# Kernel optimization log

Measured on AMD Instinct MI355X. Metric: run time of the kernel, lower is better.

The kernel has to match this reference:

```python
import jax, jax.numpy as jnp
import numpy as np
from jax import lax

B, N, C, H, W, D, BEV = 2, 6, 64, 128, 352, 48, 64


def _make_buffers():
    # depths: linspace(1,100,D) -> used with shape (1,1,D,1)
    depths = jnp.linspace(1.0, 100.0, D).reshape(1, 1, D, 1)
    y, x = jnp.meshgrid(jnp.arange(H), jnp.arange(W), indexing='ij')
    xy1 = jnp.stack((x.flatten(), y.flatten(), jnp.ones(H * W)), axis=0).astype(jnp.float32)  # (3, H*W)
    return depths, xy1


def setup_inputs() -> dict:
    key = jax.random.key(0)
    ks = jax.random.split(key, 8)
    image_features = jax.random.normal(ks[0], (B * N, C, H, W), jnp.float32)
    # realistic invertible pinhole intrinsics embedded in 4x4
    fx = 500.0 + 10.0 * jax.random.normal(ks[1], (B, N))
    fy = 500.0 + 10.0 * jax.random.normal(ks[2], (B, N))
    K = jnp.tile(jnp.eye(4, dtype=jnp.float32), (B, N, 1, 1))
    K = K.at[..., 0, 0].set(fx).at[..., 1, 1].set(fy)
    K = K.at[..., 0, 2].set(W / 2.0).at[..., 1, 2].set(H / 2.0)
    extrinsics = jnp.tile(jnp.eye(4, dtype=jnp.float32), (B, N, 1, 1)) + 0.01 * jax.random.normal(ks[3], (B, N, 4, 4))
    view_attention = jnp.ones((1, N, 1, H, W), jnp.float32)
    depth_attention = jnp.ones((1, D, 1, 1), jnp.float32)
    # kaiming-normal conv weights (fan_in mode, relu gain sqrt(2))
    c1w = jax.random.normal(ks[4], (BEV, 3, 3, 3), jnp.float32) * np.sqrt(2.0 / (3 * 9))
    c1b = jnp.zeros((BEV,), jnp.float32)
    c2w = jax.random.normal(ks[5], (BEV, BEV, 3, 3), jnp.float32) * np.sqrt(2.0 / (BEV * 9))
    c2b = jnp.zeros((BEV,), jnp.float32)
    bn1_g = jnp.ones((BEV,), jnp.float32); bn1_b = jnp.zeros((BEV,), jnp.float32)
    bn2_g = jnp.ones((BEV,), jnp.float32); bn2_b = jnp.zeros((BEV,), jnp.float32)
    depths, xy1 = _make_buffers()
    return dict(image_features=image_features, intrinsics=K, extrinsics=extrinsics,
                view_attention=view_attention, depth_attention=depth_attention,
                c1w=c1w, c1b=c1b, bn1_g=bn1_g, bn1_b=bn1_b,
                c2w=c2w, c2b=c2b, bn2_g=bn2_g, bn2_b=bn2_b,
                depths=depths, xy1=xy1)


def _conv3x3(x, w, b):
    y = lax.conv_general_dilated(x, w, (1, 1), 'SAME',
                                 dimension_numbers=('NCHW', 'OIHW', 'NCHW'))
    return y + b.reshape(1, -1, 1, 1)


def _bn_train(x, g, b, eps=1e-5):
    # torch BatchNorm2d in training mode: biased batch stats over (B,H,W)
    m = x.mean(axis=(0, 2, 3), keepdims=True)
    v = x.var(axis=(0, 2, 3), keepdims=True)
    return g.reshape(1, -1, 1, 1) * (x - m) * lax.rsqrt(v + eps) + b.reshape(1, -1, 1, 1)


def reference(image_features, intrinsics, extrinsics, view_attention, depth_attention,
              c1w, c1b, bn1_g, bn1_b, c2w, c2b, bn2_g, bn2_b, depths, xy1):
    BN = B * N
    # ---- lift ----
    K3 = intrinsics.reshape(BN, 4, 4)[:, :3, :3]
    Kinv = jnp.linalg.inv(K3)                          # (BN,3,3)
    rays = jnp.einsum('bij,jp->bip', Kinv, xy1)        # (BN,3,H*W)
    # depths (1,1,D,1) * rays (BN,3,1,HW) -> (BN,3,D,HW), then the original's
    # .view(B,N,3,H,W,D) (a raw row-major reshape, reproduced faithfully)
    pc = (depths * rays[:, :, None, :]).reshape(B, N, 3, H, W, D)
    # (depth_probs in the original is computed then discarded; omitted)
    # ---- splat (fused weighted reduction over N and D) ----
    da = jax.nn.softmax(depth_attention, axis=1).reshape(D)       # (D,)
    va = jax.nn.softmax(view_attention, axis=1)[0, :, 0]          # (N,H,W)
    bev_features = jnp.einsum('bnchwd,d,nhw->bchw', pc, da, va)   # (B,3,H,W)
    h = jax.nn.relu(_bn_train(_conv3x3(bev_features, c1w, c1b), bn1_g, bn1_b))
    bev = jax.nn.relu(_bn_train(_conv3x3(h, c2w, c2b), bn2_g, bn2_b))
    return pc, bev
```

## Files before the change

### kernel.cpp

```cpp
#include <hip/hip_runtime.h>

#define W_ 352
#define H_ 128
#define HW 45056
#define D_ 48
#define B_ 2
#define N_ 6
#define DHW (D_*HW)
#define PC_SIZE (36*DHW)
#define BHW (B_*HW)
#define BEVN (B_*64*HW)

#define WS_KINV 0
#define WS_SUM1 192
#define WS_SQ1  256
#define WS_SUM2 448
#define WS_SQ2  512

#define NBN_BLK (BEVN/2048)
#define NPC_BLK (PC_SIZE/1024)

typedef unsigned short ushort_t;
typedef __attribute__((ext_vector_type(8))) short bf16x8;
typedef __attribute__((ext_vector_type(4))) float f32x4;
typedef __attribute__((ext_vector_type(8))) unsigned short u16x8;

static __device__ inline ushort_t f2bf(float f) {
    union { float f; unsigned u; } v; v.f = f;
    unsigned r = v.u + 0x7FFF + ((v.u >> 16) & 1);
    return (ushort_t)(r >> 16);
}
static __device__ inline float bf2f(ushort_t u) {
    union { unsigned u; float f; } v; v.u = ((unsigned)u) << 16; return v.f;
}
static __device__ inline void invert3x3(const float* __restrict__ M, float* __restrict__ o) {
    float a = M[0], b = M[1], c = M[2];
    float d = M[4], e = M[5], f = M[6];
    float g = M[8], h = M[9], ii = M[10];
    float det = a*(e*ii - f*h) - b*(d*ii - f*g) + c*(d*h - e*g);
    float inv = 1.f / det;
    o[0] = (e*ii - f*h)*inv; o[1] = (c*h - b*ii)*inv; o[2] = (b*f - c*e)*inv;
    o[3] = (f*g - d*ii)*inv; o[4] = (a*ii - c*g)*inv; o[5] = (c*d - a*f)*inv;
    o[6] = (d*h - e*g)*inv;  o[7] = (b*g - a*h)*inv;  o[8] = (a*e - b*d)*inv;
}

static __device__ inline void pc_write(int pcblk, const float* __restrict__ ws,
                                       const float* __restrict__ depths,
                                       float* __restrict__ out) {
    int f = pcblk * 1024 + (int)threadIdx.x * 4;
    int bnc = f / DHW;
    int r1  = f - bnc * DHW;
    int d   = r1 / HW;
    int p   = r1 - d * HW;
    int y   = p / W_;
    int x   = p - y * W_;
    float ka = ws[WS_KINV + bnc * 3 + 0];
    float kb = ws[WS_KINV + bnc * 3 + 1];
    float kc = ws[WS_KINV + bnc * 3 + 2];
    float dep = depths[d];
    float base = fmaf(kb, (float)y, kc);
    f32x4 v;
    v.x = dep * fmaf(ka, (float)(x + 0), base);
    v.y = dep * fmaf(ka, (float)(x + 1), base);
    v.z = dep * fmaf(ka, (float)(x + 2), base);
    v.w = dep * fmaf(ka, (float)(x + 3), base);
    __builtin_nontemporal_store(v, (f32x4*)(out + f));
}

__global__ __launch_bounds__(256) void k_fused1(const float* __restrict__ K4,
                                                const float* __restrict__ datt,
                                                const float* __restrict__ vatt,
                                                const float* __restrict__ depths,
                                                const float* __restrict__ w1,
                                                const float* __restrict__ b1,
                                                const float* __restrict__ w2,
                                                float* __restrict__ ws,
                                                ushort_t* __restrict__ h1pm,
                                                ushort_t* __restrict__ packedW) {
    int bid = blockIdx.x, tid = threadIdx.x;
    if (bid >= 352) {
        int e = (bid - 352) * 256 + tid;
        int tap = e >> 12;
        int r   = e & 4095;
        int n   = r >> 6, k = r & 63;
        int slot = (k >> 3) ^ (n & 7);
        packedW[tap * 4096 + n * 64 + slot * 8 + (k & 7)] = f2bf(w2[(n * 64 + k) * 9 + tap]);
        return;
    }
    if (bid == 0) {
        for (int i = 192 + tid; i < 576; i += 256) ws[i] = 0.f;
        if (tid >= 128 && tid < 140)
            invert3x3(K4 + (tid - 128) * 16, ws + WS_KINV + (tid - 128) * 9);
    }
    __shared__ float sBev[3][10][34];
    __shared__ float wl[64 * 27];
    __shared__ float sDep[48], sDa[48], sKinv[54];

    int b  = bid / 176;
    int t0 = bid - b * 176;
    int ty = t0 / 11, tx = t0 - ty * 11;
    int y0 = ty * 8, x0 = tx * 32;

    if (tid < 48) sDep[tid] = depths[tid];
    if (tid >= 64 && tid < 70) invert3x3(K4 + (b * 6 + tid - 64) * 16, sKinv + (tid - 64) * 9);
    if (tid == 192) {
        float mx = -1e30f;
        for (int k = 0; k < D_; k++) mx = fmaxf(mx, datt[k]);
        float s = 0.f, e[D_];
        for (int k = 0; k < D_; k++) { e[k] = expf(datt[k] - mx); s += e[k]; }
        float invs = 1.f / s;
        for (int k = 0; k < D_; k++) sDa[k] = e[k] * invs;
    }
    for (int i = tid; i < 64 * 27; i += 256) wl[i] = w1[i];
    __syncthreads();

    for (int idx = tid; idx < 340; idx += 256) {
        int hy = idx / 34, hx = idx - hy * 34;
        int py = y0 + hy - 1, px = x0 + hx - 1;
        float a0 = 0.f, a1 = 0.f, a2 = 0.f;
        if ((unsigned)py < H_ && (unsigned)px < W_) {
            int pix = py * W_ + px;
            float va[N_]; float mx = -1e30f;
            for (int n = 0; n < N_; n++) { va[n] = vatt[n * HW + pix]; mx = fmaxf(mx, va[n]); }
            float s = 0.f;
            for (int n = 0; n < N_; n++) { va[n] = expf(va[n] - mx); s += va[n]; }
            float invs = 1.f / s;
            int q0 = pix * 48;
            int d = q0 / HW;
            int p = q0 - d * HW;
            int y = p / W_;
            int x = p - y * W_;
            float fx = (float)x, fy = (float)y;
            float S0 = 0.f, S1 = 0.f, S2 = 0.f;
            #pragma unroll
            for (int dd = 0; dd < D_; dd++) {
                float wq = sDa[dd] * sDep[d];
                S0 = fmaf(wq, fx, S0);
                S1 = fmaf(wq, fy, S1);
                S2 += wq;
                x++; fx += 1.f;
                if (x == W_) { x = 0; fx = 0.f; y++; fy += 1.f; if (y == H_) { y = 0; fy = 0.f; d++; } }
            }
            for (int n = 0; n < N_; n++) {
                float van = va[n] * invs;
                const float* kv = sKinv + n * 9;
                a0 = fmaf(van, fmaf(kv[0], S0, fmaf(kv[1], S1, kv[2] * S2)), a0);
                a1 = fmaf(van, fmaf(kv[3], S0, fmaf(kv[4], S1, kv[5] * S2)), a1);
                a2 = fmaf(van, fmaf(kv[6], S0, fmaf(kv[7], S1, kv[8] * S2)), a2);
            }
        }
        sBev[0][hy][hx] = a0;
        sBev[1][hy][hx] = a1;
        sBev[2][hy][hx] = a2;
    }
    __syncthreads();

    int oy = tid >> 5, ox = tid & 31;
    int y = y0 + oy, x = x0 + ox;
    float v[27];
    #pragma unroll
    for (int ci = 0; ci < 3; ci++)
        #pragma unroll
        for (int dy = 0; dy < 3; dy++)
            #pragma unroll
            for (int dx = 0; dx < 3; dx++)
                v[ci * 9 + dy * 3 + dx] = sBev[ci][oy + dy][ox + dx];
    u16x8 pack[8];
    #pragma unroll
    for (int co = 0; co < 64; co++) {
        float acc = b1[co];
        #pragma unroll
        for (int k = 0; k < 27; k++) acc = fmaf(wl[co * 27 + k], v[k], acc);
        pack[co >> 3][co & 7] = (short)f2bf(acc);
    }
    ushort_t* dst = h1pm + (size_t)(b * HW + y * W_ + x) * 64;
    #pragma unroll
    for (int j = 0; j < 8; j++)
        *(u16x8*)(dst + j * 8) = pack[j];
}

__global__ __launch_bounds__(256) void k_stats(const ushort_t* __restrict__ x,
                                               float* __restrict__ ws) {
    __shared__ float sSum[64], sSq[64];
    int tid = threadIdx.x;
    if (tid < 64) { sSum[tid] = 0.f; sSq[tid] = 0.f; }
    __syncthreads();
    int c8 = tid & 7;
    int lp = tid >> 3;
    int base = blockIdx.x * 352;
    float s[8] = {0,0,0,0,0,0,0,0}, q[8] = {0,0,0,0,0,0,0,0};
    for (int p = lp; p < 352; p += 32) {
        u16x8 v = *(const u16x8*)(x + (size_t)(base + p) * 64 + c8 * 8);
        #pragma unroll
        for (int e = 0; e < 8; e++) {
            float f = bf2f(v[e]);
            s[e] += f;
            q[e] = fmaf(f, f, q[e]);
        }
    }
    #pragma unroll
    for (int e = 0; e < 8; e++) {
        s[e] += __shfl_xor(s[e], 8);  s[e] += __shfl_xor(s[e], 16); s[e] += __shfl_xor(s[e], 32);
        q[e] += __shfl_xor(q[e], 8);  q[e] += __shfl_xor(q[e], 16); q[e] += __shfl_xor(q[e], 32);
    }
    if ((tid & 56) == 0) {
        #pragma unroll
        for (int e = 0; e < 8; e++) {
            atomicAdd(&sSum[c8 * 8 + e], s[e]);
            atomicAdd(&sSq[c8 * 8 + e], q[e]);
        }
    }
    __syncthreads();
    if (tid < 64) {
        atomicAdd(ws + WS_SUM1 + tid, sSum[tid]);
        atomicAdd(ws + WS_SQ1 + tid, sSq[tid]);
    }
}

__global__ __launch_bounds__(256) void k_conv2(const ushort_t* __restrict__ h1pm,
                                               const ushort_t* __restrict__ packedW,
                                               const float* __restrict__ b2,
                                               const float* __restrict__ g1,
                                               const float* __restrict__ bb1,
                                               float* __restrict__ ws,
                                               float* __restrict__ h2f) {
    __shared__ __align__(16) ushort_t sA[204 * 64];
    __shared__ __align__(16) ushort_t sB[3 * 4096];
    __shared__ float sSc[64], sSh[64];
    __shared__ float sRs[4][64], sRq[4][64];

    const int tid = threadIdx.x;
    if (tid < 64) {
        const float invM = 1.f / (float)BHW;
        float m = ws[WS_SUM1 + tid] * invM;
        float var = ws[WS_SQ1 + tid] * invM - m * m;
        float sc = g1[tid] * rsqrtf(var + 1e-5f);
        sSc[tid] = sc;
        sSh[tid] = bb1[tid] - m * sc;
    }
    __syncthreads();

    const int bid = blockIdx.x;
    const int b  = bid / 352;
    const int r0 = bid - b * 352;
    const int yb = r0 / 11;
    const int xb = r0 - yb * 11;
    const int x0 = xb * 32;
    const int y0 = yb * 4;
    const ushort_t* h1p = h1pm + (size_t)b * HW * 64;

    for (int idx = tid; idx < 204 * 8; idx += 256) {
        int r  = idx >> 3;
        int c8 = idx & 7;
        int hy = r / 34;
        int hx = r - hy * 34;
        int py = y0 + hy - 1, px = x0 + hx - 1;
        u16x8 ov = {0, 0, 0, 0, 0, 0, 0, 0};
        if ((unsigned)py < H_ && (unsigned)px < W_) {
            u16x8 v = *(const u16x8*)(h1p + (size_t)(py * W_ + px) * 64 + c8 * 8);
            #pragma unroll
            for (int e = 0; e < 8; e++) {
                int ci = c8 * 8 + e;
                float f = fmaxf(fmaf(sSc[ci], bf2f(v[e]), sSh[ci]), 0.f);
                ov[e] = (short)f2bf(f);
            }
        }
        int slot = c8 ^ (r & 7);
        *(u16x8*)(&sA[r * 64 + slot * 8]) = ov;
    }

    const int w    = tid >> 6;
    const int lane = tid & 63;
    const int g    = lane >> 4;
    const int c16  = lane & 15;

    f32x4 acc[2][4];
    #pragma unroll
    for (int m = 0; m < 2; m++)
        #pragma unroll
        for (int n = 0; n < 4; n++)
            acc[m][n] = (f32x4){0.f, 0.f, 0.f, 0.f};

    for (int grp = 0; grp < 3; grp++) {
        __syncthreads();
        const uint4* src = (const uint4*)(packedW + grp * 3 * 4096);
        uint4* dst = (uint4*)sB;
        #pragma unroll
        for (int i = 0; i < 6; i++) dst[tid + 256 * i] = src[tid + 256 * i];
        __syncthreads();
        #pragma unroll
        for (int tt = 0; tt < 3; tt++) {
            bf16x8 afr[2][2];
            #pragma unroll
            for (int mrep = 0; mrep < 2; mrep++)
                #pragma unroll
                for (int kk = 0; kk < 2; kk++) {
                    int r = (w + grp) * 34 + tt + c16 + 16 * mrep;
                    int slot = (g + 4 * kk) ^ (r & 7);
                    afr[mrep][kk] = *(const bf16x8*)(&sA[r * 64 + slot * 8]);
                }
            #pragma unroll
            for (int nrep = 0; nrep < 4; nrep++) {
                int n = 16 * nrep + c16;
                #pragma unroll
                for (int kk = 0; kk < 2; kk++) {
                    int slot = (g + 4 * kk) ^ (n & 7);
                    bf16x8 bfr = *(const bf16x8*)(&sB[tt * 4096 + n * 64 + slot * 8]);
                    #pragma unroll
                    for (int mrep = 0; mrep < 2; mrep++)
                        acc[mrep][nrep] = __builtin_amdgcn_mfma_f32_16x16x32_bf16(
                            afr[mrep][kk], bfr, acc[mrep][nrep], 0, 0, 0);
                }
            }
        }
    }

    const int y = y0 + w;
    #pragma unroll
    for (int nrep = 0; nrep < 4; nrep++) {
        int co = 16 * nrep + c16;
        float bias = b2[co];
        float* dstrow = h2f + (size_t)(b * 64 + co) * HW + y * W_;
        float s = 0.f, q = 0.f;
        #pragma unroll
        for (int mrep = 0; mrep < 2; mrep++)
            #pragma unroll
            for (int j = 0; j < 4; j++) {
                float val = acc[mrep][nrep][j] + bias;
                s += val;
                q = fmaf(val, val, q);
                dstrow[x0 + 16 * mrep + g * 4 + j] = val;
            }
        s += __shfl_xor(s, 16); s += __shfl_xor(s, 32);
        q += __shfl_xor(q, 16); q += __shfl_xor(q, 32);
        if (g == 0) { sRs[w][co] = s; sRq[w][co] = q; }
    }
    __syncthreads();
    if (tid < 64) {
        float s = sRs[0][tid] + sRs[1][tid] + sRs[2][tid] + sRs[3][tid];
        float q = sRq[0][tid] + sRq[1][tid] + sRq[2][tid] + sRq[3][tid];
        atomicAdd(ws + WS_SUM2 + tid, s);
        atomicAdd(ws + WS_SQ2 + tid, q);
    }
}

__global__ __launch_bounds__(256) void k_tail(const float* __restrict__ depths,
                                              const float* __restrict__ ws,
                                              const float* __restrict__ g2,
                                              const float* __restrict__ bb2,
                                              float* __restrict__ out) {
    int bid = blockIdx.x;
    if (bid >= NBN_BLK) { pc_write(bid - NBN_BLK, ws, depths, out); return; }
    float* bev = out + PC_SIZE;
    int t = bid * 256 + threadIdx.x;
    int f = t * 8;
    int c = (f / HW) & 63;
    const float invM = 1.f / (float)BHW;
    float m = ws[WS_SUM2 + c] * invM;
    float var = ws[WS_SQ2 + c] * invM - m * m;
    float sc = g2[c] * rsqrtf(var + 1e-5f);
    float sh = bb2[c] - m * sc;
    f32x4 a = *(f32x4*)(bev + f);
    f32x4 d = *(f32x4*)(bev + f + 4);
    a.x = fmaxf(fmaf(sc, a.x, sh), 0.f);
    a.y = fmaxf(fmaf(sc, a.y, sh), 0.f);
    a.z = fmaxf(fmaf(sc, a.z, sh), 0.f);
    a.w = fmaxf(fmaf(sc, a.w, sh), 0.f);
    d.x = fmaxf(fmaf(sc, d.x, sh), 0.f);
    d.y = fmaxf(fmaf(sc, d.y, sh), 0.f);
    d.z = fmaxf(fmaf(sc, d.z, sh), 0.f);
    d.w = fmaxf(fmaf(sc, d.w, sh), 0.f);
    *(f32x4*)(bev + f) = a;
    *(f32x4*)(bev + f + 4) = d;
}

extern "C" void kernel_launch(void* const* d_in, const int* in_sizes, int n_in,
                              void* d_out, int out_size, void* d_ws, size_t ws_size,
                              hipStream_t stream) {
    const float* K4     = (const float*)d_in[1];
    const float* vatt   = (const float*)d_in[3];
    const float* datt   = (const float*)d_in[4];
    const float* c1w    = (const float*)d_in[5];
    const float* c1b    = (const float*)d_in[6];
    const float* g1     = (const float*)d_in[7];
    const float* bb1    = (const float*)d_in[8];
    const float* c2w    = (const float*)d_in[9];
    const float* c2b    = (const float*)d_in[10];
    const float* g2     = (const float*)d_in[11];
    const float* bb2    = (const float*)d_in[12];
    const float* depths = (const float*)d_in[13];

    float* out = (float*)d_out;
    float* ws  = (float*)d_ws;
    char* base = (char*)d_out;
    ushort_t* h1pm    = (ushort_t*)base;
    ushort_t* packedW = (ushort_t*)(base + (12u << 20));
    float*    h2f     = out + PC_SIZE;

    k_fused1<<<496, 256, 0, stream>>>(K4, datt, vatt, depths, c1w, c1b, c2w, ws, h1pm, packedW);
    k_stats <<<256, 256, 0, stream>>>(h1pm, ws);
    k_conv2 <<<704, 256, 0, stream>>>(h1pm, packedW, c2b, g1, bb1, ws, h2f);
    k_tail  <<<NBN_BLK + NPC_BLK, 256, 0, stream>>>(depths, ws, g2, bb2, out);
}
```

Before: 124.5 us.

## Fuse BN1 statistics into conv1 kernel and loop the point-cloud writer

Conv1 output is now also staged in shared memory, and each block reduces its own per-channel sum and sum-of-squares, so the separate k_stats kernel and its re-read of h1pm go away. The ws accumulators are now zeroed with hipMemsetAsync before the first kernel, because blocks accumulate into them concurrently. The point-cloud write in k_tail now has each block loop over 18 chunks with plain stores instead of launching one block per chunk with nontemporal stores. The cost is 32 KB of extra shared memory in k_fused1, which may cut occupancy, plus an extra memset call in the stream.

```diff
diff --git a/kernel.cpp b/kernel.cpp
--- a/kernel.cpp
+++ b/kernel.cpp
@@ -18,7 +18,8 @@
 #define WS_SQ2  512
 
 #define NBN_BLK (BEVN/2048)
-#define NPC_BLK (PC_SIZE/1024)
+#define NPC_BLK 4224
+#define PC_ITER 18
 
 typedef unsigned short ushort_t;
 typedef __attribute__((ext_vector_type(8))) short bf16x8;
@@ -42,29 +43,6 @@
     o[0] = (e*ii - f*h)*inv; o[1] = (c*h - b*ii)*inv; o[2] = (b*f - c*e)*inv;
     o[3] = (f*g - d*ii)*inv; o[4] = (a*ii - c*g)*inv; o[5] = (c*d - a*f)*inv;
     o[6] = (d*h - e*g)*inv;  o[7] = (b*g - a*h)*inv;  o[8] = (a*e - b*d)*inv;
-}
-
-static __device__ inline void pc_write(int pcblk, const float* __restrict__ ws,
-                                       const float* __restrict__ depths,
-                                       float* __restrict__ out) {
-    int f = pcblk * 1024 + (int)threadIdx.x * 4;
-    int bnc = f / DHW;
-    int r1  = f - bnc * DHW;
-    int d   = r1 / HW;
-    int p   = r1 - d * HW;
-    int y   = p / W_;
-    int x   = p - y * W_;
-    float ka = ws[WS_KINV + bnc * 3 + 0];
-    float kb = ws[WS_KINV + bnc * 3 + 1];
-    float kc = ws[WS_KINV + bnc * 3 + 2];
-    float dep = depths[d];
-    float base = fmaf(kb, (float)y, kc);
-    f32x4 v;
-    v.x = dep * fmaf(ka, (float)(x + 0), base);
-    v.y = dep * fmaf(ka, (float)(x + 1), base);
-    v.z = dep * fmaf(ka, (float)(x + 2), base);
-    v.w = dep * fmaf(ka, (float)(x + 3), base);
-    __builtin_nontemporal_store(v, (f32x4*)(out + f));
 }
 
 __global__ __launch_bounds__(256) void k_fused1(const float* __restrict__ K4,
@@ -87,14 +65,14 @@
         packedW[tap * 4096 + n * 64 + slot * 8 + (k & 7)] = f2bf(w2[(n * 64 + k) * 9 + tap]);
         return;
     }
-    if (bid == 0) {
-        for (int i = 192 + tid; i < 576; i += 256) ws[i] = 0.f;
-        if (tid >= 128 && tid < 140)
-            invert3x3(K4 + (tid - 128) * 16, ws + WS_KINV + (tid - 128) * 9);
-    }
+    if (bid == 0 && tid >= 128 && tid < 140)
+        invert3x3(K4 + (tid - 128) * 16, ws + WS_KINV + (tid - 128) * 9);
+
     __shared__ float sBev[3][10][34];
     __shared__ float wl[64 * 27];
     __shared__ float sDep[48], sDa[48], sKinv[54];
+    __shared__ __align__(16) ushort_t sTile[256 * 64];
+    __shared__ float sSum[64], sSq[64];
 
     int b  = bid / 176;
     int t0 = bid - b * 176;
@@ -102,6 +80,7 @@
     int y0 = ty * 8, x0 = tx * 32;
 
     if (tid < 48) sDep[tid] = depths[tid];
+    if (tid < 64) { sSum[tid] = 0.f; sSq[tid] = 0.f; }
     if (tid >= 64 && tid < 70) invert3x3(K4 + (b * 6 + tid - 64) * 16, sKinv + (tid - 64) * 9);
     if (tid == 192) {
         float mx = -1e30f;
@@ -175,25 +154,20 @@
     }
     ushort_t* dst = h1pm + (size_t)(b * HW + y * W_ + x) * 64;
     #pragma unroll
-    for (int j = 0; j < 8; j++)
+    for (int j = 0; j < 8; j++) {
         *(u16x8*)(dst + j * 8) = pack[j];
-}
-
-__global__ __launch_bounds__(256) void k_stats(const ushort_t* __restrict__ x,
-                                               float* __restrict__ ws) {
-    __shared__ float sSum[64], sSq[64];
-    int tid = threadIdx.x;
-    if (tid < 64) { sSum[tid] = 0.f; sSq[tid] = 0.f; }
-    __syncthreads();
+        *(u16x8*)(&sTile[tid * 64 + j * 8]) = pack[j];
+    }
+    __syncthreads();
+
     int c8 = tid & 7;
     int lp = tid >> 3;
-    int base = blockIdx.x * 352;
     float s[8] = {0,0,0,0,0,0,0,0}, q[8] = {0,0,0,0,0,0,0,0};
-    for (int p = lp; p < 352; p += 32) {
-        u16x8 v = *(const u16x8*)(x + (size_t)(base + p) * 64 + c8 * 8);
+    for (int p = lp; p < 256; p += 32) {
+        u16x8 vv = *(const u16x8*)(&sTile[p * 64 + c8 * 8]);
         #pragma unroll
         for (int e = 0; e < 8; e++) {
-            float f = bf2f(v[e]);
+            float f = bf2f(vv[e]);
             s[e] += f;
             q[e] = fmaf(f, f, q[e]);
         }
@@ -349,10 +323,34 @@
                                               const float* __restrict__ g2,
                                               const float* __restrict__ bb2,
                                               float* __restrict__ out) {
-    int bid = blockIdx.x;
-    if (bid >= NBN_BLK) { pc_write(bid - NBN_BLK, ws, depths, out); return; }
+    int bid = blockIdx.x, tid = threadIdx.x;
+    if (bid >= NBN_BLK) {
+        int pcbid = bid - NBN_BLK;
+        for (int i = 0; i < PC_ITER; i++) {
+            int ch = i * NPC_BLK + pcbid;
+            int f = ch * 1024 + tid * 4;
+            int bnc = f / DHW;
+            int r1  = f - bnc * DHW;
+            int d   = r1 / HW;
+            int p   = r1 - d * HW;
+            int y   = p / W_;
+            int x   = p - y * W_;
+            float ka = ws[WS_KINV + bnc * 3 + 0];
+            float kb = ws[WS_KINV + bnc * 3 + 1];
+            float kc = ws[WS_KINV + bnc * 3 + 2];
+            float dep = depths[d];
+            float base = fmaf(kb, (float)y, kc);
+            f32x4 v;
+            v.x = dep * fmaf(ka, (float)(x + 0), base);
+            v.y = dep * fmaf(ka, (float)(x + 1), base);
+            v.z = dep * fmaf(ka, (float)(x + 2), base);
+            v.w = dep * fmaf(ka, (float)(x + 3), base);
+            *(f32x4*)(out + f) = v;
+        }
+        return;
+    }
     float* bev = out + PC_SIZE;
-    int t = bid * 256 + threadIdx.x;
+    int t = bid * 256 + tid;
     int f = t * 8;
     int c = (f / HW) & 63;
     const float invM = 1.f / (float)BHW;
@@ -397,8 +395,8 @@
     ushort_t* packedW = (ushort_t*)(base + (12u << 20));
     float*    h2f     = out + PC_SIZE;
 
+    hipMemsetAsync(ws, 0, 640 * sizeof(float), stream);
     k_fused1<<<496, 256, 0, stream>>>(K4, datt, vatt, depths, c1w, c1b, c2w, ws, h1pm, packedW);
-    k_stats <<<256, 256, 0, stream>>>(h1pm, ws);
     k_conv2 <<<704, 256, 0, stream>>>(h1pm, packedW, c2b, g1, bb1, ws, h2f);
     k_tail  <<<NBN_BLK + NPC_BLK, 256, 0, stream>>>(depths, ws, g2, bb2, out);
 }
```

New measurement: 137.1 us. +10.1%, slower.
